# Performance work log

Measured on AMD Instinct MI355X. Metric: run time of the kernel, lower is better.

## Reference

```python
import jax, jax.numpy as jnp
import numpy as np

GLOBAL = 3
BETA = 10
CR, CO, CS = 9, 2, 1
N_PCA = 45
PARENTS = [0, 1, 2, 0, 4, 5, 0, 7, 8, 0, 10, 11, 0, 13, 14]
JOINT_REORDER_MESH = {4: 743, 8: 333, 12: 443, 16: 555, 20: 678}


def rodrigues(r):
    # r: [..., 3] axis-angle -> [..., 3, 3] rotation matrix
    theta = jnp.sqrt(jnp.sum(r * r, axis=-1, keepdims=True) + 1e-8)
    n = r / theta
    th = theta[..., None]
    c, s = jnp.cos(th), jnp.sin(th)
    nx, ny, nz = n[..., 0], n[..., 1], n[..., 2]
    z = jnp.zeros_like(nx)
    K = jnp.stack([z, -nz, ny, nz, z, -nx, -ny, nx, z], axis=-1).reshape(r.shape[:-1] + (3, 3))
    outer = n[..., :, None] * n[..., None, :]
    eye = jnp.eye(3, dtype=r.dtype)
    return c * eye + (1.0 - c) * outer + s * K


def setup_inputs() -> dict:
    key = jax.random.key(0)
    ks = jax.random.split(key, 12)
    B, T, D = 32, 128, 5376
    out_dim = N_PCA + GLOBAL + BETA + CR + CO + CS  # 70
    return {
        "x": jax.random.normal(ks[0], (B, T, D), dtype=jnp.float32),
        "W": jax.random.normal(ks[1], (out_dim, D), dtype=jnp.float32) * 0.01,
        "b": jax.random.normal(ks[2], (out_dim,), dtype=jnp.float32) * 0.01,
        "hand_ppal_comps": jax.random.normal(ks[3], (N_PCA, 45), dtype=jnp.float32) * 0.1,
        "mean_hand": jax.random.normal(ks[4], (45,), dtype=jnp.float32) * 0.1,
        "hand_template": jax.random.normal(ks[5], (778, 3), dtype=jnp.float32) * 0.05,
        "shapedirs": jax.random.normal(ks[6], (778, 3, 10), dtype=jnp.float32) * 0.01,
        "posedirs": jax.random.normal(ks[7], (778, 3, 135), dtype=jnp.float32) * 0.01,
        "J_reg": jax.random.uniform(ks[8], (16, 778), dtype=jnp.float32) / 778.0,
        "lbs_weights": jax.nn.softmax(jax.random.normal(ks[9], (778, 16), dtype=jnp.float32), axis=-1),
    }


def _forward(x, W, b, hand_ppal_comps, mean_hand, hand_template, shapedirs, posedirs, J_reg, lbs_weights):
    N, T, _ = x.shape
    params = x @ W.T + b  # [N,T,70]
    n_pca = hand_ppal_comps.shape[0]
    off = GLOBAL + n_pca
    theta = params[..., :off]
    beta = params[..., off:off + BETA]
    c_r = params[..., off + BETA:off + BETA + CR]
    c_o = params[..., off + BETA + CR:off + BETA + CR + CO]
    c_s = params[..., off + BETA + CR + CO:off + BETA + CR + CO + CS]

    # pose from PCA
    hand_posed = theta[..., GLOBAL:] @ hand_ppal_comps + mean_hand  # [N,T,45]
    hand_posed = jnp.concatenate([theta[..., :GLOBAL], hand_posed], axis=-1)  # [N,T,48]

    # shape blendshapes and joints
    hand_shaped = jnp.einsum('vck,btk->btvc', shapedirs, beta) + hand_template  # [N,T,778,3]
    J = jnp.einsum('jv,btvc->btjc', J_reg, hand_shaped)  # [N,T,16,3]

    # pose blendshapes (lrotmin: flattened Rodrigues matrices of the 15 finger joints)
    rod135 = rodrigues(hand_posed[..., GLOBAL:].reshape(N, T, 15, 3)).reshape(N, T, 135)
    curr_hand = hand_shaped + jnp.einsum('vck,btk->btvc', posedirs, rod135)

    # global rigid transformation (kinematic tree)
    rot16 = rodrigues(hand_posed.reshape(N, T, 16, 3))  # [N,T,16,3,3]
    row = jnp.broadcast_to(jnp.array([0.0, 0.0, 0.0, 1.0], dtype=x.dtype), (N, T, 1, 4))
    T0 = jnp.concatenate([jnp.concatenate([rot16[:, :, 0], J[:, :, 0, :, None]], axis=-1), row], axis=-2)  # [N,T,4,4]
    parents = np.array(PARENTS)
    rel = (J[:, :, 1:] - J[:, :, parents])[..., None]  # [N,T,15,3,1]
    op = jnp.concatenate([rot16[:, :, 1:], rel], axis=-1)  # [N,T,15,3,4]
    row15 = jnp.broadcast_to(jnp.array([0.0, 0.0, 0.0, 1.0], dtype=x.dtype), (N, T, 15, 1, 4))
    op = jnp.concatenate([op, row15], axis=-2)  # [N,T,15,4,4]
    res = [T0]
    for i in range(15):
        res.append(res[PARENTS[i]] @ op[:, :, i])
    results = jnp.stack(res, axis=2)  # [N,T,16,4,4]

    ext_J = jnp.concatenate([J, jnp.zeros((N, T, 16, 1), dtype=x.dtype)], axis=-1)
    corr = jnp.einsum('btjik,btjk->btji', results, ext_J)  # [N,T,16,4]
    A = results - jnp.concatenate([jnp.zeros((N, T, 16, 4, 3), dtype=x.dtype), corr[..., None]], axis=-1)
    J3d = results[..., :3, 3]  # [N,T,16,3]

    # linear blend skinning
    Tv = jnp.einsum('btjik,vj->btvik', A, lbs_weights)  # [N,T,778,4,4]
    curr_h = jnp.concatenate([curr_hand, jnp.ones((N, T, 778, 1), dtype=x.dtype)], axis=-1)
    mesh = jnp.einsum('btvij,btvj->btvi', Tv, curr_h)[..., :3]  # [N,T,778,3]

    jr = lambda i: J3d[:, :, i]
    mv = lambda v: mesh[:, :, v]
    J3d_re = jnp.stack([jr(0), jr(13), jr(14), jr(15), mv(743), jr(1), jr(2), jr(3), mv(333),
                        jr(4), jr(5), jr(6), mv(443), jr(10), jr(11), jr(12), mv(555),
                        jr(7), jr(8), jr(9), mv(678)], axis=2)  # [N,T,21,3]

    c_r3 = c_r.reshape(N, T, 3, 3)
    J2d = (J3d_re @ c_r3)[..., :2]
    J2d = c_s[:, :, None] * J2d + c_o[:, :, None]
    return (J2d, theta, beta)


def reference(x, W, b, hand_ppal_comps, mean_hand, hand_template, shapedirs, posedirs, J_reg, lbs_weights):
    return _forward(x, W, b, hand_ppal_comps, mean_hand, hand_template, shapedirs, posedirs, J_reg, lbs_weights)
```

## Files before the change

### kernel.cpp

```cpp
#include <hip/hip_runtime.h>
#include <hip/hip_bf16.h>

typedef short short8 __attribute__((ext_vector_type(8)));
typedef float float4_ __attribute__((ext_vector_type(4)));
typedef unsigned short ushort_t;

#define OUT_THETA 172032
#define OUT_BETA  368640
#define NROW 4096
#define KDIM 5376
#define NPAD 80

#define WFRAG_OFF 0
#define PART_OFF  860160
#define JSD_OFF   6103040
#define JT_OFF    6104960
#define PSEL_OFF  6105152
#define SSEL_OFF  6113252
#define TSEL_OFF  6113852
#define WSEL_OFF  6113912

__device__ __constant__ int c_jslot[16] = {0,5,6,7,9,10,11,17,18,19,13,14,15,1,2,3};
__device__ __constant__ int c_vslot[5]  = {4,8,12,16,20};

__device__ inline short f2bf(float f) {
  union { float f; unsigned u; } v; v.f = f;
  unsigned r = v.u + 0x7fffu + ((v.u >> 16) & 1u);
  return (short)(r >> 16);
}

__device__ inline short8 cvt8(float4_ a, float4_ b) {
  short8 r;
  r[0]=f2bf(a[0]); r[1]=f2bf(a[1]); r[2]=f2bf(a[2]); r[3]=f2bf(a[3]);
  r[4]=f2bf(b[0]); r[5]=f2bf(b[1]); r[6]=f2bf(b[2]); r[7]=f2bf(b[3]);
  return r;
}

__global__ __launch_bounds__(256) void setup_kernel(
    const float* __restrict__ W, const float* __restrict__ shapedirs,
    const float* __restrict__ posedirs, const float* __restrict__ Jreg,
    const float* __restrict__ tmpl, const float* __restrict__ lbs,
    ushort_t* __restrict__ wfrag, float* __restrict__ jsd, float* __restrict__ jt,
    float* __restrict__ psel, float* __restrict__ ssel, float* __restrict__ tsel,
    float* __restrict__ wsel)
{
  int b = blockIdx.x, t = threadIdx.x;
  if (b < 1680) {
    int idx = b*256 + t;
    int n = idx / KDIM, k = idx % KDIM;
    float v = (n < 70) ? W[(size_t)n*KDIM + k] : 0.f;
    wfrag[((size_t)(k>>3)*NPAD + n)*8 + (k&7)] = (ushort_t)f2bf(v);
  } else if (b < 1812) {
    int wv = (b-1680)*4 + (t>>6);
    int l = t & 63;
    float p = 0.f;
    if (wv < 480) {
      int j = wv/30, r = wv%30, c = r/10, kk = r%10;
      for (int v = l; v < 778; v += 64) p += Jreg[j*778+v]*shapedirs[(v*3+c)*10+kk];
    } else {
      int o = wv-480; int j = o/3, c = o%3;
      for (int v = l; v < 778; v += 64) p += Jreg[j*778+v]*tmpl[v*3+c];
    }
    for (int off = 32; off > 0; off >>= 1) p += __shfl_down(p, off);
    if (l == 0) { if (wv < 480) jsd[wv] = p; else jt[wv-480] = p; }
  } else {
    const int vtx[5] = {743,333,443,555,678};
    for (int s = t; s < 2270; s += 256) {
      if (s < 2025) { int vi = s/405, r = s%405, c = r/135, kk = r%135;
        psel[s] = posedirs[((size_t)vtx[vi]*3 + c)*135 + kk]; }
      else if (s < 2175) { int u = s-2025; int vi = u/30, r = u%30, c = r/10, kk = r%10;
        ssel[u] = shapedirs[((size_t)vtx[vi]*3 + c)*10 + kk]; }
      else if (s < 2190) { int u = s-2175; int vi = u/3, c = u%3;
        tsel[u] = tmpl[vtx[vi]*3 + c]; }
      else if (s < 2270) { int u = s-2190; int vi = u/16, j = u%16;
        wsel[u] = lbs[vtx[vi]*16 + j]; }
    }
  }
}

__global__ __launch_bounds__(256) void gemm_params(
    const float* __restrict__ x, const ushort_t* __restrict__ wfrag,
    float* __restrict__ part)
{
  const int KQ = 1344, NCH = KQ/32;
  int gw = (blockIdx.x << 2) + (threadIdx.x >> 6);
  int l = threadIdx.x & 63;
  int nt = gw % 5;
  int rg = (gw / 5) & 255;
  int kq = gw / (5*256);
  int m0 = rg << 4, n0 = nt << 4, k0 = kq * KQ;
  int q = l >> 4, lm = l & 15;

  const float* ap = x + (size_t)(m0 + lm)*KDIM + k0 + q*8;
  const ushort_t* bp = wfrag + ((size_t)((k0>>3) + q)*NPAD + n0 + lm)*8;
  float4_ acc = {0.f,0.f,0.f,0.f};
  #pragma unroll 2
  for (int c = 0; c < NCH; ++c) {
    float4_ a0 = *(const float4_*)ap;
    float4_ a1 = *(const float4_*)(ap+4);
    short8 bfr = *(const short8*)bp;
    short8 afr = cvt8(a0, a1);
    acc = __builtin_amdgcn_mfma_f32_16x16x32_bf16(afr, bfr, acc, 0, 0, 0);
    ap += 32; bp += 4*NPAD*8;
  }
  float* op = part + ((size_t)(kq*NROW) + m0)*NPAD + n0 + lm;
  #pragma unroll
  for (int r = 0; r < 4; ++r) op[(size_t)(q*4 + r)*NPAD] = acc[r];
}

__global__ __launch_bounds__(64) void decode_kernel(
    const float* __restrict__ part, const float* __restrict__ bvec,
    const float* __restrict__ comps, const float* __restrict__ meanh,
    const float* __restrict__ jsd, const float* __restrict__ jt,
    const float* __restrict__ psel, const float* __restrict__ ssel,
    const float* __restrict__ tsel, const float* __restrict__ wsel,
    float* __restrict__ out)
{
  int row = blockIdx.x;
  int l = threadIdx.x;
  __shared__ float P[70];
  __shared__ float HP[48];
  __shared__ float R[16][9];
  __shared__ float Jl[48];
  __shared__ float RES[16][16];
  __shared__ float Al[16][16];
  __shared__ float CH[5][4];
  __shared__ float M3[21][3];

  {
    float v = part[(size_t)row*NPAD + l]
            + part[(size_t)(NROW+row)*NPAD + l]
            + part[(size_t)(2*NROW+row)*NPAD + l]
            + part[(size_t)(3*NROW+row)*NPAD + l] + bvec[l];
    P[l] = v;
    if (l < 48) out[OUT_THETA + (size_t)row*48 + l] = v;
    else if (l < 58) out[OUT_BETA + (size_t)row*10 + (l-48)] = v;
    if (l < 6) {
      int c2 = l + 64;
      P[c2] = part[(size_t)row*NPAD + c2]
            + part[(size_t)(NROW+row)*NPAD + c2]
            + part[(size_t)(2*NROW+row)*NPAD + c2]
            + part[(size_t)(3*NROW+row)*NPAD + c2] + bvec[c2];
    }
  }
  __syncthreads();

  if (l < 45) {
    float s = meanh[l];
    for (int k = 0; k < 45; ++k) s += P[3+k]*comps[k*45 + l];
    HP[3+l] = s;
  } else if (l < 48) HP[l-45] = P[l-45];
  __syncthreads();

  if (l < 16) {
    float rx = HP[3*l], ry = HP[3*l+1], rz = HP[3*l+2];
    float th = sqrtf(rx*rx + ry*ry + rz*rz + 1e-8f);
    float inv = 1.0f/th;
    float nx = rx*inv, ny = ry*inv, nz = rz*inv;
    float cth = cosf(th), sth = sinf(th), mc = 1.0f - cth;
    R[l][0] = cth + mc*nx*nx;     R[l][1] = mc*nx*ny - sth*nz;  R[l][2] = mc*nx*nz + sth*ny;
    R[l][3] = mc*ny*nx + sth*nz;  R[l][4] = cth + mc*ny*ny;     R[l][5] = mc*ny*nz - sth*nx;
    R[l][6] = mc*nz*nx - sth*ny;  R[l][7] = mc*nz*ny + sth*nx;  R[l][8] = cth + mc*nz*nz;
  }
  if (l < 48) {
    float s = jt[l];
    #pragma unroll
    for (int k = 0; k < 10; ++k) s += jsd[l*10+k]*P[48+k];
    Jl[l] = s;
  }
  __syncthreads();

  if (l < 16) {
    int r = l >> 2, c = l & 3;
    RES[0][l] = (r < 3) ? ((c < 3) ? R[0][3*r+c] : Jl[r]) : ((c == 3) ? 1.f : 0.f);
  }
  __syncthreads();
  constexpr int PARS[15] = {0,1,2,0,4,5,0,7,8,0,10,11,0,13,14};
  #pragma unroll
  for (int i = 0; i < 15; ++i) {
    const int p = PARS[i];
    if (l < 16) {
      int r = l >> 2, c = l & 3;
      float s = (c == 3) ? RES[p][4*r+3] : 0.f;
      #pragma unroll
      for (int k = 0; k < 3; ++k) {
        float opv = (c < 3) ? R[i+1][3*k+c] : (Jl[3*(i+1)+k] - Jl[3*p+k]);
        s += RES[p][4*r+k]*opv;
      }
      RES[i+1][l] = s;
    }
    __syncthreads();
  }

  {
    int j = l >> 2, r = l & 3;
    float corr = RES[j][4*r]*Jl[3*j] + RES[j][4*r+1]*Jl[3*j+1] + RES[j][4*r+2]*Jl[3*j+2];
    Al[j][4*r+0] = RES[j][4*r+0];
    Al[j][4*r+1] = RES[j][4*r+1];
    Al[j][4*r+2] = RES[j][4*r+2];
    Al[j][4*r+3] = RES[j][4*r+3] - corr;
  }
  if (l < 15) {
    int vi = l/3, ci = l%3;
    float s = tsel[l];
    #pragma unroll
    for (int k = 0; k < 10; ++k) s += ssel[l*10+k]*P[48+k];
    for (int j15 = 0; j15 < 15; ++j15) {
      #pragma unroll
      for (int e = 0; e < 9; ++e) s += psel[l*135 + j15*9 + e]*R[j15+1][e];
    }
    CH[vi][ci] = s;
  }
  __syncthreads();

  if (l < 48) {
    int j = l/3, c = l%3;
    M3[c_jslot[j]][c] = RES[j][4*c+3];
  } else if (l < 63) {
    int s0 = l - 48; int vi = s0/3, r = s0%3;
    float m = 0.f;
    #pragma unroll
    for (int j = 0; j < 16; ++j) {
      float tv = Al[j][4*r]*CH[vi][0] + Al[j][4*r+1]*CH[vi][1]
               + Al[j][4*r+2]*CH[vi][2] + Al[j][4*r+3];
      m += wsel[vi*16+j]*tv;
    }
    M3[c_vslot[vi]][r] = m;
  }
  __syncthreads();

  if (l < 42) {
    int k = l >> 1, d = l & 1;
    float s = M3[k][0]*P[58 + d] + M3[k][1]*P[58 + 3 + d] + M3[k][2]*P[58 + 6 + d];
    out[((size_t)row*21 + k)*2 + d] = P[69]*s + P[67+d];
  }
}

extern "C" void kernel_launch(void* const* d_in, const int* in_sizes, int n_in,
                              void* d_out, int out_size, void* d_ws, size_t ws_size,
                              hipStream_t stream) {
  const float* x         = (const float*)d_in[0];
  const float* W         = (const float*)d_in[1];
  const float* bvec      = (const float*)d_in[2];
  const float* comps     = (const float*)d_in[3];
  const float* meanh     = (const float*)d_in[4];
  const float* tmpl      = (const float*)d_in[5];
  const float* shapedirs = (const float*)d_in[6];
  const float* posedirs  = (const float*)d_in[7];
  const float* Jreg      = (const float*)d_in[8];
  const float* lbs       = (const float*)d_in[9];

  char* ws = (char*)d_ws;
  ushort_t* wfrag = (ushort_t*)(ws + WFRAG_OFF);
  float* part = (float*)(ws + PART_OFF);
  float* jsd  = (float*)(ws + JSD_OFF);
  float* jt   = (float*)(ws + JT_OFF);
  float* psel = (float*)(ws + PSEL_OFF);
  float* ssel = (float*)(ws + SSEL_OFF);
  float* tsel = (float*)(ws + TSEL_OFF);
  float* wsel = (float*)(ws + WSEL_OFF);
  float* out  = (float*)d_out;

  hipLaunchKernelGGL(setup_kernel, dim3(1813), dim3(256), 0, stream,
                     W, shapedirs, posedirs, Jreg, tmpl, lbs,
                     wfrag, jsd, jt, psel, ssel, tsel, wsel);
  hipLaunchKernelGGL(gemm_params, dim3(1280), dim3(256), 0, stream, x, wfrag, part);
  hipLaunchKernelGGL(decode_kernel, dim3(4096), dim3(64), 0, stream,
                     part, bvec, comps, meanh, jsd, jt, psel, ssel, tsel, wsel, out);
}
```

Before: 203.7 us.

## Compute all N tiles per wave to reuse x loads, adaptive split-K, vectorized W pack

The GEMM now has each wave compute all five 16-column N tiles. Each x fragment is loaded and converted to bf16 once instead of five times, and the loads for the next K chunk are issued before the current MFMAs run. The split-K factor is chosen at runtime from the workspace size (4, 6 or 12), and the workspace layout and decode reduction are changed to match. Weight packing now converts eight elements per thread with vector loads and stores. The costs are more registers per wave, fewer waves when KS is small, and a longer partial-sum reduction in decode when KS is large.

```diff
diff --git a/kernel.cpp b/kernel.cpp
--- a/kernel.cpp
+++ b/kernel.cpp
@@ -10,15 +10,6 @@
 #define NROW 4096
 #define KDIM 5376
 #define NPAD 80
-
-#define WFRAG_OFF 0
-#define PART_OFF  860160
-#define JSD_OFF   6103040
-#define JT_OFF    6104960
-#define PSEL_OFF  6105152
-#define SSEL_OFF  6113252
-#define TSEL_OFF  6113852
-#define WSEL_OFF  6113912
 
 __device__ __constant__ int c_jslot[16] = {0,5,6,7,9,10,11,17,18,19,13,14,15,1,2,3};
 __device__ __constant__ int c_vslot[5]  = {4,8,12,16,20};
@@ -45,13 +36,21 @@
     float* __restrict__ wsel)
 {
   int b = blockIdx.x, t = threadIdx.x;
-  if (b < 1680) {
+  if (b < 210) {
     int idx = b*256 + t;
-    int n = idx / KDIM, k = idx % KDIM;
-    float v = (n < 70) ? W[(size_t)n*KDIM + k] : 0.f;
-    wfrag[((size_t)(k>>3)*NPAD + n)*8 + (k&7)] = (ushort_t)f2bf(v);
-  } else if (b < 1812) {
-    int wv = (b-1680)*4 + (t>>6);
+    int n = idx / 672, kg = idx % 672;
+    short8 o;
+    if (n < 70) {
+      const float* wp = W + (size_t)n*KDIM + kg*8;
+      float4_ w0 = *(const float4_*)wp;
+      float4_ w1 = *(const float4_*)(wp+4);
+      o = cvt8(w0, w1);
+    } else {
+      o = (short8){0,0,0,0,0,0,0,0};
+    }
+    *(short8*)(wfrag + ((size_t)kg*NPAD + n)*8) = o;
+  } else if (b < 342) {
+    int wv = (b-210)*4 + (t>>6);
     int l = t & 63;
     float p = 0.f;
     if (wv < 480) {
@@ -80,32 +79,65 @@
 
 __global__ __launch_bounds__(256) void gemm_params(
     const float* __restrict__ x, const ushort_t* __restrict__ wfrag,
-    float* __restrict__ part)
+    float* __restrict__ part, int nchunk)
 {
-  const int KQ = 1344, NCH = KQ/32;
   int gw = (blockIdx.x << 2) + (threadIdx.x >> 6);
   int l = threadIdx.x & 63;
-  int nt = gw % 5;
-  int rg = (gw / 5) & 255;
-  int kq = gw / (5*256);
-  int m0 = rg << 4, n0 = nt << 4, k0 = kq * KQ;
+  int rg = gw & 255;
+  int kq = gw >> 8;
+  int m0 = rg << 4;
+  int k0 = kq * (nchunk << 5);
   int q = l >> 4, lm = l & 15;
 
   const float* ap = x + (size_t)(m0 + lm)*KDIM + k0 + q*8;
-  const ushort_t* bp = wfrag + ((size_t)((k0>>3) + q)*NPAD + n0 + lm)*8;
-  float4_ acc = {0.f,0.f,0.f,0.f};
-  #pragma unroll 2
-  for (int c = 0; c < NCH; ++c) {
-    float4_ a0 = *(const float4_*)ap;
-    float4_ a1 = *(const float4_*)(ap+4);
-    short8 bfr = *(const short8*)bp;
-    short8 afr = cvt8(a0, a1);
-    acc = __builtin_amdgcn_mfma_f32_16x16x32_bf16(afr, bfr, acc, 0, 0, 0);
+  const ushort_t* bp = wfrag + ((size_t)((k0>>3) + q)*NPAD + lm)*8;
+
+  float4_ acc0 = {0.f,0.f,0.f,0.f}, acc1 = acc0, acc2 = acc0, acc3 = acc0, acc4 = acc0;
+
+  float4_ a0 = *(const float4_*)ap;
+  float4_ a1 = *(const float4_*)(ap+4);
+  short8 b0 = *(const short8*)(bp);
+  short8 b1 = *(const short8*)(bp+128);
+  short8 b2 = *(const short8*)(bp+256);
+  short8 b3 = *(const short8*)(bp+384);
+  short8 b4 = *(const short8*)(bp+512);
+  ap += 32; bp += 4*NPAD*8;
+
+  for (int c = 0; c < nchunk-1; ++c) {
+    float4_ na0 = *(const float4_*)ap;
+    float4_ na1 = *(const float4_*)(ap+4);
+    short8 nb0 = *(const short8*)(bp);
+    short8 nb1 = *(const short8*)(bp+128);
+    short8 nb2 = *(const short8*)(bp+256);
+    short8 nb3 = *(const short8*)(bp+384);
+    short8 nb4 = *(const short8*)(bp+512);
     ap += 32; bp += 4*NPAD*8;
-  }
-  float* op = part + ((size_t)(kq*NROW) + m0)*NPAD + n0 + lm;
+    short8 af = cvt8(a0, a1);
+    acc0 = __builtin_amdgcn_mfma_f32_16x16x32_bf16(af, b0, acc0, 0, 0, 0);
+    acc1 = __builtin_amdgcn_mfma_f32_16x16x32_bf16(af, b1, acc1, 0, 0, 0);
+    acc2 = __builtin_amdgcn_mfma_f32_16x16x32_bf16(af, b2, acc2, 0, 0, 0);
+    acc3 = __builtin_amdgcn_mfma_f32_16x16x32_bf16(af, b3, acc3, 0, 0, 0);
+    acc4 = __builtin_amdgcn_mfma_f32_16x16x32_bf16(af, b4, acc4, 0, 0, 0);
+    a0 = na0; a1 = na1; b0 = nb0; b1 = nb1; b2 = nb2; b3 = nb3; b4 = nb4;
+  }
+  {
+    short8 af = cvt8(a0, a1);
+    acc0 = __builtin_amdgcn_mfma_f32_16x16x32_bf16(af, b0, acc0, 0, 0, 0);
+    acc1 = __builtin_amdgcn_mfma_f32_16x16x32_bf16(af, b1, acc1, 0, 0, 0);
+    acc2 = __builtin_amdgcn_mfma_f32_16x16x32_bf16(af, b2, acc2, 0, 0, 0);
+    acc3 = __builtin_amdgcn_mfma_f32_16x16x32_bf16(af, b3, acc3, 0, 0, 0);
+    acc4 = __builtin_amdgcn_mfma_f32_16x16x32_bf16(af, b4, acc4, 0, 0, 0);
+  }
+
+  float* op = part + ((size_t)kq*NROW + m0 + q*4)*NPAD + lm;
   #pragma unroll
-  for (int r = 0; r < 4; ++r) op[(size_t)(q*4 + r)*NPAD] = acc[r];
+  for (int r = 0; r < 4; ++r) {
+    op[(size_t)r*NPAD +  0] = acc0[r];
+    op[(size_t)r*NPAD + 16] = acc1[r];
+    op[(size_t)r*NPAD + 32] = acc2[r];
+    op[(size_t)r*NPAD + 48] = acc3[r];
+    op[(size_t)r*NPAD + 64] = acc4[r];
+  }
 }
 
 __global__ __launch_bounds__(64) void decode_kernel(
@@ -114,7 +146,7 @@
     const float* __restrict__ jsd, const float* __restrict__ jt,
     const float* __restrict__ psel, const float* __restrict__ ssel,
     const float* __restrict__ tsel, const float* __restrict__ wsel,
-    float* __restrict__ out)
+    float* __restrict__ out, int KS)
 {
   int row = blockIdx.x;
   int l = threadIdx.x;
@@ -128,19 +160,16 @@
   __shared__ float M3[21][3];
 
   {
-    float v = part[(size_t)row*NPAD + l]
-            + part[(size_t)(NROW+row)*NPAD + l]
-            + part[(size_t)(2*NROW+row)*NPAD + l]
-            + part[(size_t)(3*NROW+row)*NPAD + l] + bvec[l];
+    float v = bvec[l];
+    for (int k = 0; k < KS; ++k) v += part[((size_t)k*NROW + row)*NPAD + l];
     P[l] = v;
     if (l < 48) out[OUT_THETA + (size_t)row*48 + l] = v;
     else if (l < 58) out[OUT_BETA + (size_t)row*10 + (l-48)] = v;
     if (l < 6) {
       int c2 = l + 64;
-      P[c2] = part[(size_t)row*NPAD + c2]
-            + part[(size_t)(NROW+row)*NPAD + c2]
-            + part[(size_t)(2*NROW+row)*NPAD + c2]
-            + part[(size_t)(3*NROW+row)*NPAD + c2] + bvec[c2];
+      float w = bvec[c2];
+      for (int k = 0; k < KS; ++k) w += part[((size_t)k*NROW + row)*NPAD + c2];
+      P[c2] = w;
     }
   }
   __syncthreads();
@@ -250,21 +279,30 @@
   const float* Jreg      = (const float*)d_in[8];
   const float* lbs       = (const float*)d_in[9];
 
+  const size_t PART_ONE = (size_t)NROW*NPAD*4;
+  const size_t TAIL = 860160 + 1920 + 192 + 8100 + 600 + 60 + 320;
+  int KS = 4;
+  if (ws_size >= 12*PART_ONE + TAIL) KS = 12;
+  else if (ws_size >= 6*PART_ONE + TAIL) KS = 6;
+  const int nchunk = 168 / KS;
+
   char* ws = (char*)d_ws;
-  ushort_t* wfrag = (ushort_t*)(ws + WFRAG_OFF);
-  float* part = (float*)(ws + PART_OFF);
-  float* jsd  = (float*)(ws + JSD_OFF);
-  float* jt   = (float*)(ws + JT_OFF);
-  float* psel = (float*)(ws + PSEL_OFF);
-  float* ssel = (float*)(ws + SSEL_OFF);
-  float* tsel = (float*)(ws + TSEL_OFF);
-  float* wsel = (float*)(ws + WSEL_OFF);
+  float*    part  = (float*)ws;
+  ushort_t* wfrag = (ushort_t*)(ws + KS*PART_ONE);
+  char*     tb    = ws + KS*PART_ONE + 860160;
+  float* jsd  = (float*)tb;
+  float* jt   = (float*)(tb + 1920);
+  float* psel = (float*)(tb + 1920 + 192);
+  float* ssel = (float*)(tb + 1920 + 192 + 8100);
+  float* tsel = (float*)(tb + 1920 + 192 + 8100 + 600);
+  float* wsel = (float*)(tb + 1920 + 192 + 8100 + 600 + 60);
   float* out  = (float*)d_out;
 
-  hipLaunchKernelGGL(setup_kernel, dim3(1813), dim3(256), 0, stream,
+  hipLaunchKernelGGL(setup_kernel, dim3(343), dim3(256), 0, stream,
                      W, shapedirs, posedirs, Jreg, tmpl, lbs,
                      wfrag, jsd, jt, psel, ssel, tsel, wsel);
-  hipLaunchKernelGGL(gemm_params, dim3(1280), dim3(256), 0, stream, x, wfrag, part);
+  hipLaunchKernelGGL(gemm_params, dim3(64*KS), dim3(256), 0, stream,
+                     x, wfrag, part, nchunk);
   hipLaunchKernelGGL(decode_kernel, dim3(4096), dim3(64), 0, stream,
-                     part, bvec, comps, meanh, jsd, jt, psel, ssel, tsel, wsel, out);
-}
+                     part, bvec, comps, meanh, jsd, jt, psel, ssel, tsel, wsel, out, KS);
+}
```

After: 182.7 us. 1.12x faster.
